# Kernel tuning notes

Hardware: AMD Instinct MI355X
Metric: run time of the kernel (lower is better)

The kernel has to match this reference:

```python
import jax, jax.numpy as jnp
import numpy as np

NUM_HEADS = 12


def setup_inputs() -> dict:
    key = jax.random.key(0)
    ks = jax.random.split(key, 12)
    B, S, H = 8, 1024, 768
    h = jax.random.normal(ks[0], (B, S, H), dtype=jnp.float32)
    att_bias = jax.random.normal(ks[1], (B, S, S, NUM_HEADS), dtype=jnp.float32)
    mask = jax.random.randint(ks[2], (B, S, S), 0, 2, dtype=jnp.int32)
    sc = 1.0 / np.sqrt(H)
    Wq = jax.random.normal(ks[3], (H, H), dtype=jnp.float32) * sc
    bq = jax.random.normal(ks[4], (H,), dtype=jnp.float32) * 0.01
    Wk = jax.random.normal(ks[5], (H, H), dtype=jnp.float32) * sc
    bk = jax.random.normal(ks[6], (H,), dtype=jnp.float32) * 0.01
    Wv = jax.random.normal(ks[7], (H, H), dtype=jnp.float32) * sc
    bv = jax.random.normal(ks[8], (H,), dtype=jnp.float32) * 0.01
    Wo = jax.random.normal(ks[9], (H, H), dtype=jnp.float32) * sc
    bo = jax.random.normal(ks[10], (H,), dtype=jnp.float32) * 0.01
    return {"h": h, "att_bias": att_bias, "mask": mask,
            "Wq": Wq, "bq": bq, "Wk": Wk, "bk": bk,
            "Wv": Wv, "bv": bv, "Wo": Wo, "bo": bo}


def reference(h, att_bias, mask, Wq, bq, Wk, bk, Wv, bv, Wo, bo):
    B, S, H = h.shape
    nh = NUM_HEADS
    d = H // nh
    scale = d ** -0.5
    # projections -> [B, nh, S, d]
    q = (h @ Wq + bq).reshape(B, S, nh, d).transpose(0, 2, 1, 3)
    k = (h @ Wk + bk).reshape(B, S, nh, d).transpose(0, 2, 1, 3)
    v = (h @ Wv + bv).reshape(B, S, nh, d).transpose(0, 2, 1, 3)
    # scores [B, nh, S, S] + additive bias (permuted from [B,S,S,nh])
    scores = jnp.einsum('bhqd,bhkd->bhqk', q, k) * scale
    scores = scores + att_bias.transpose(0, 3, 1, 2)
    # masked_fill with 1e-14 (faithful to original: near-zero score, not -inf)
    scores = jnp.where(mask[:, None, :, :].astype(bool),
                       jnp.asarray(1e-14, scores.dtype), scores)
    attn = jax.nn.softmax(scores, axis=-1)  # dropout p=0 -> identity
    out = jnp.einsum('bhqk,bhkd->bhqd', attn, v)
    out = out.transpose(0, 2, 1, 3).reshape(B, S, H)
    return out @ Wo + bo
```

## Files before the change

kernel.cpp:

```cpp
#include <hip/hip_runtime.h>


typedef __attribute__((ext_vector_type(8))) __bf16 bf16x8;
typedef __attribute__((ext_vector_type(4))) __bf16 bf16x4;
typedef __attribute__((ext_vector_type(4))) float floatx4;
typedef __attribute__((ext_vector_type(4))) short short4v;
using bf16 = __bf16;

#define HID 768
#define NHEAD 12
#define DHEAD 64
#define SEQ 1024
#define NBATCH 8
#define WELEM (HID * HID)
#define QKVELEM (NBATCH * NHEAD * SEQ * DHEAD)
#define OPELEM QKVELEM
#define MLROWS (NBATCH * NHEAD * SEQ)

__device__ __forceinline__ floatx4 mfma_bf16(bf16x8 a, bf16x8 b, floatx4 c) {
  return __builtin_amdgcn_mfma_f32_16x16x32_bf16(a, b, c, 0, 0, 0);
}

__device__ __forceinline__ floatx4 mfma16_bf16(bf16x4 a, bf16x4 b, floatx4 c) {
#if __has_builtin(__builtin_amdgcn_mfma_f32_16x16x16bf16_1k)
  return __builtin_amdgcn_mfma_f32_16x16x16bf16_1k(
      __builtin_bit_cast(short4v, a), __builtin_bit_cast(short4v, b), c, 0, 0, 0);
#else
  floatx4 d = c;
  asm volatile("s_nop 1\n\tv_mfma_f32_16x16x16_bf16 %0, %1, %2, %0\n\ts_nop 4"
               : "+v"(d) : "v"(a), "v"(b));
  return d;
#endif
}

#define ASYNC16(gp, lp)                                           \
  __builtin_amdgcn_global_load_lds(                               \
      (__attribute__((address_space(1))) void*)(gp),              \
      (__attribute__((address_space(3))) void*)(lp), 16, 0, 0)

__global__ void prep_weights(const float* __restrict__ Wq, const float* __restrict__ Wk,
                             const float* __restrict__ Wv, const float* __restrict__ Wo,
                             bf16* __restrict__ WT) {
  __shared__ float t[32][33];
  const int m = blockIdx.z;
  const float* W = (m == 0) ? Wq : (m == 1) ? Wk : (m == 2) ? Wv : Wo;
  const int k0 = blockIdx.x * 32, n0 = blockIdx.y * 32;
  const int tx = threadIdx.x, ty = threadIdx.y;
#pragma unroll
  for (int i = 0; i < 4; ++i)
    t[ty + 8 * i][tx] = W[(size_t)(k0 + ty + 8 * i) * HID + n0 + tx];
  __syncthreads();
  bf16* o = WT + (size_t)m * WELEM;
#pragma unroll
  for (int i = 0; i < 4; ++i)
    o[(size_t)(n0 + ty + 8 * i) * HID + k0 + tx] = (bf16)t[tx][ty + 8 * i];
}

__global__ void prep_h(const float* __restrict__ X, bf16* __restrict__ Y) {
  const size_t i = ((size_t)blockIdx.x * 256 + threadIdx.x) * 8;
  float4 a = *(const float4*)(X + i);
  float4 b = *(const float4*)(X + i + 4);
  bf16x8 o;
  o[0] = (bf16)a.x; o[1] = (bf16)a.y; o[2] = (bf16)a.z; o[3] = (bf16)a.w;
  o[4] = (bf16)b.x; o[5] = (bf16)b.y; o[6] = (bf16)b.z; o[7] = (bf16)b.w;
  *(bf16x8*)(Y + i) = o;
}

__launch_bounds__(256, 2)
__global__ void qkv_gemm(const bf16* __restrict__ A, const bf16* __restrict__ WT,
                         const float* __restrict__ bq, const float* __restrict__ bk,
                         const float* __restrict__ bv,
                         bf16* __restrict__ Qb, bf16* __restrict__ Kb,
                         bf16* __restrict__ Vb) {
  __shared__ __align__(16) bf16 As[128][32];
  __shared__ __align__(16) bf16 Bs[128][32];
  const int mat = blockIdx.z;
  const int bn = blockIdx.x * 128, bm = blockIdx.y * 128;
  const bf16* W = WT + (size_t)mat * WELEM;
  const int tid = threadIdx.x, lane = tid & 63, warp = tid >> 6;
  const int fr = lane & 15, quad = lane >> 4;
  const int wr = warp >> 1, wc = warp & 1;

  floatx4 acc[4][4] = {};

  const int srow = tid >> 2, scol = (tid & 3) * 8;
  const bf16* as0 = A + (size_t)(bm + srow) * HID + scol;
  const bf16* as1 = A + (size_t)(bm + 64 + srow) * HID + scol;
  const bf16* bs0 = W + (size_t)(bn + srow) * HID + scol;
  const bf16* bs1 = W + (size_t)(bn + 64 + srow) * HID + scol;
  bf16* la0 = &As[srow][scol];
  bf16* la1 = &As[64 + srow][scol];
  bf16* lb0 = &Bs[srow][scol];
  bf16* lb1 = &Bs[64 + srow][scol];

  for (int k0 = 0; k0 < HID; k0 += 32) {
    ASYNC16(as0 + k0, la0);
    ASYNC16(as1 + k0, la1);
    ASYNC16(bs0 + k0, lb0);
    ASYNC16(bs1 + k0, lb1);
    __syncthreads();
    bf16x8 a[4], b[4];
#pragma unroll
    for (int mi = 0; mi < 4; ++mi) a[mi] = *(const bf16x8*)&As[wr * 64 + mi * 16 + fr][quad * 8];
#pragma unroll
    for (int ni = 0; ni < 4; ++ni) b[ni] = *(const bf16x8*)&Bs[wc * 64 + ni * 16 + fr][quad * 8];
#pragma unroll
    for (int mi = 0; mi < 4; ++mi)
#pragma unroll
      for (int ni = 0; ni < 4; ++ni) acc[mi][ni] = mfma_bf16(a[mi], b[ni], acc[mi][ni]);
    __syncthreads();
  }

  const float* bias = (mat == 0) ? bq : (mat == 1) ? bk : bv;
#pragma unroll
  for (int mi = 0; mi < 4; ++mi)
#pragma unroll
    for (int ni = 0; ni < 4; ++ni)
#pragma unroll
      for (int r = 0; r < 4; ++r) {
        const int grow = bm + wr * 64 + mi * 16 + quad * 4 + r;
        const int gcol = bn + wc * 64 + ni * 16 + fr;
        float v = acc[mi][ni][r] + bias[gcol];
        const int bb = grow >> 10, ss = grow & 1023;
        const int head = gcol >> 6, dc = gcol & 63;
        const size_t bh = (size_t)bb * NHEAD + head;
        const size_t idx = (bh * SEQ + ss) * DHEAD + dc;
        if (mat == 0) Qb[idx] = (bf16)(v * 0.125f);
        else if (mat == 1) Kb[idx] = (bf16)v;
        else Vb[idx] = (bf16)v;
      }
}

__global__ void vtrans(const bf16* __restrict__ Vb, bf16* __restrict__ Vt) {
  __shared__ bf16 t[64][72];
  const int st = blockIdx.x, bh = blockIdx.y;
  const int tid = threadIdx.x;
  const bf16* src = Vb + ((size_t)bh * SEQ + st * 64) * DHEAD;
#pragma unroll
  for (int p = 0; p < 2; ++p) {
    const int r = p * 32 + (tid >> 3), c = (tid & 7) * 8;
    *(bf16x8*)&t[r][c] = *(const bf16x8*)(src + (size_t)r * DHEAD + c);
  }
  __syncthreads();
#pragma unroll
  for (int p = 0; p < 2; ++p) {
    const int d = p * 32 + (tid >> 3), s0 = (tid & 7) * 8;
    bf16x8 o;
#pragma unroll
    for (int k = 0; k < 8; ++k) o[k] = t[s0 + k][d];
    *(bf16x8*)(Vt + ((size_t)bh * DHEAD + d) * SEQ + st * 64 + s0) = o;
  }
}

__launch_bounds__(256, 4)
__global__ void attn_kernel(const bf16* __restrict__ Qb, const bf16* __restrict__ Kb,
                            const bf16* __restrict__ Vt, const float* __restrict__ bias,
                            const int* __restrict__ maskp,
                            float* __restrict__ Op, float2* __restrict__ Ml) {
  __shared__ __align__(16) float4 BbU[1536];
  __shared__ __align__(16) int4  MbU[128];

  const int qt = blockIdx.x, b = blockIdx.y, ks = blockIdx.z;
  const int tid = threadIdx.x, lane = tid & 63, warp = tid >> 6;
  const int fr = lane & 15, quad = lane >> 4;
  const size_t brow = (size_t)b * SEQ + qt * 16;

  float* Opk = Op + (size_t)ks * OPELEM;
  float2* Mlk = Ml + (size_t)ks * MLROWS;

  bf16x8 qa0[3], qa1[3];
#pragma unroll
  for (int j = 0; j < 3; ++j) {
    const size_t bh = (size_t)b * NHEAD + 3 * warp + j;
    const bf16* Qp = Qb + (bh * SEQ + qt * 16) * DHEAD;
    qa0[j] = *(const bf16x8*)(Qp + fr * DHEAD + quad * 8);
    qa1[j] = *(const bf16x8*)(Qp + fr * DHEAD + 32 + quad * 8);
  }

  const float4* bias4 = (const float4*)bias;
  const float4* bsrc[6];
#pragma unroll
  for (int i = 0; i < 6; ++i) {
    const int f = tid + 256 * i, q = f / 96, rl = f % 96;
    const int rg = (rl & ~7) | ((rl ^ q) & 7);
    bsrc[i] = bias4 + ((size_t)(brow + q) * SEQ) * 3 + rg;
  }
  const int4* msrc = nullptr;
  if (tid < 128) {
    const int q = tid >> 3, s = tid & 7;
    msrc = (const int4*)(maskp + (size_t)(brow + q) * SEQ) + (s ^ (q & 7));
  }

  float mrun[3] = {-1e30f, -1e30f, -1e30f};
  float lrun[3] = {0.f, 0.f, 0.f};
  floatx4 oaccT[3][4] = {};

  for (int ch = 0; ch < 16; ++ch) {
    const int c0 = (ks * 16 + ch) * 32;

#pragma unroll
    for (int i = 0; i < 6; ++i) ASYNC16(bsrc[i] + c0 * 3, BbU + tid + 256 * i);
    if (tid < 128) ASYNC16(msrc + c0 / 4, MbU + tid);
    __syncthreads();

    floatx4 st[3][2];
#pragma unroll
    for (int j = 0; j < 3; ++j) {
      const size_t bh = (size_t)b * NHEAD + 3 * warp + j;
#pragma unroll
      for (int ct = 0; ct < 2; ++ct) {
        const bf16* kp = Kb + (bh * SEQ + c0 + ct * 16 + fr) * DHEAD;
        bf16x8 k0 = *(const bf16x8*)(kp + quad * 8);
        bf16x8 k1 = *(const bf16x8*)(kp + 32 + quad * 8);
        floatx4 t = {0.f, 0.f, 0.f, 0.f};
        t = mfma_bf16(k0, qa0[j], t);
        t = mfma_bf16(k1, qa1[j], t);
        st[j][ct] = t;
      }
    }

    const float* Bf = (const float*)BbU;
#pragma unroll
    for (int ct = 0; ct < 2; ++ct) {
      const int4 m4 = MbU[fr * 8 + ((ct * 4 + quad) ^ (fr & 7))];
      const int mm[4] = {m4.x, m4.y, m4.z, m4.w};
#pragma unroll
      for (int r = 0; r < 4; ++r) {
        const int ug = 3 * (ct * 16 + quad * 4 + r);
        const int u0 = fr * 96 + ((ug & ~7) | ((ug ^ fr) & 7));
        const int u1 = fr * 96 + (((ug + 1) & ~7) | (((ug + 1) ^ fr) & 7));
        const int u2 = fr * 96 + (((ug + 2) & ~7) | (((ug + 2) ^ fr) & 7));
        float b0, b1, b2;
        if (warp == 0)      { const float* p = Bf + 4 * u0; b0 = p[0]; b1 = p[1]; b2 = p[2]; }
        else if (warp == 1) { const float* p = Bf + 4 * u1; b0 = Bf[4 * u0 + 3]; b1 = p[0]; b2 = p[1]; }
        else if (warp == 2) { const float* p = Bf + 4 * u1; b0 = p[2]; b1 = p[3]; b2 = Bf[4 * u2]; }
        else                { const float* p = Bf + 4 * u2; b0 = p[1]; b1 = p[2]; b2 = p[3]; }
        if (mm[r]) {
          st[0][ct][r] = 0.f; st[1][ct][r] = 0.f; st[2][ct][r] = 0.f;
        } else {
          st[0][ct][r] += b0; st[1][ct][r] += b1; st[2][ct][r] += b2;
        }
      }
    }

#pragma unroll
    for (int j = 0; j < 3; ++j) {
      float s8[8];
#pragma unroll
      for (int ct = 0; ct < 2; ++ct)
#pragma unroll
        for (int r = 0; r < 4; ++r) s8[ct * 4 + r] = st[j][ct][r];
      float mx = mrun[j];
#pragma unroll
      for (int k = 0; k < 8; ++k) mx = fmaxf(mx, s8[k]);
      mx = fmaxf(mx, __shfl_xor(mx, 16));
      mx = fmaxf(mx, __shfl_xor(mx, 32));
      const float alpha = __expf(mrun[j] - mx);
      float e[8], sum = 0.f;
#pragma unroll
      for (int k = 0; k < 8; ++k) { e[k] = __expf(s8[k] - mx); sum += e[k]; }
      sum += __shfl_xor(sum, 16);
      sum += __shfl_xor(sum, 32);
      lrun[j] = lrun[j] * alpha + sum;
      mrun[j] = mx;
      bf16x4 pa0, pa1;
#pragma unroll
      for (int r = 0; r < 4; ++r) { pa0[r] = (bf16)e[r]; pa1[r] = (bf16)e[4 + r]; }
#pragma unroll
      for (int dvt = 0; dvt < 4; ++dvt)
#pragma unroll
        for (int r = 0; r < 4; ++r) oaccT[j][dvt][r] *= alpha;
      const size_t bh = (size_t)b * NHEAD + 3 * warp + j;
#pragma unroll
      for (int dvt = 0; dvt < 4; ++dvt) {
        const bf16* vp = Vt + (bh * DHEAD + dvt * 16 + fr) * SEQ + c0 + quad * 4;
        bf16x4 v0 = *(const bf16x4*)vp;
        bf16x4 v1 = *(const bf16x4*)(vp + 16);
        oaccT[j][dvt] = mfma16_bf16(v0, pa0, oaccT[j][dvt]);
        oaccT[j][dvt] = mfma16_bf16(v1, pa1, oaccT[j][dvt]);
      }
    }

    __syncthreads();
  }

#pragma unroll
  for (int j = 0; j < 3; ++j) {
    const int hh = 3 * warp + j;
    const size_t row = ((size_t)b * NHEAD + hh) * SEQ + qt * 16 + fr;
#pragma unroll
    for (int dvt = 0; dvt < 4; ++dvt)
      *(floatx4*)(Opk + row * DHEAD + dvt * 16 + quad * 4) = oaccT[j][dvt];
    if (quad == 0) Mlk[row] = make_float2(mrun[j], lrun[j]);
  }
}

__global__ void kmerge(const float* __restrict__ O0, const float* __restrict__ O1,
                       const float2* __restrict__ ml0, const float2* __restrict__ ml1,
                       bf16* __restrict__ Ob) {
  const int t = blockIdx.x * 256 + threadIdx.x;
  const int row = t >> 4;
  const int dq = (t & 15) * 4;
  const float2 a = ml0[row], c = ml1[row];
  const float M = fmaxf(a.x, c.x);
  const float w0 = __expf(a.x - M), w1 = __expf(c.x - M);
  const float inv = 1.0f / (a.y * w0 + c.y * w1);
  floatx4 o0 = *(const floatx4*)(O0 + (size_t)row * DHEAD + dq);
  floatx4 o1 = *(const floatx4*)(O1 + (size_t)row * DHEAD + dq);
  const int bh = row >> 10, s = row & 1023;
  const int bb = bh / NHEAD, hh = bh % NHEAD;
  bf16x4 o;
#pragma unroll
  for (int r = 0; r < 4; ++r) o[r] = (bf16)((o0[r] * w0 + o1[r] * w1) * inv);
  *(bf16x4*)(Ob + ((size_t)bb * SEQ + s) * HID + hh * DHEAD + dq) = o;
}

__launch_bounds__(256, 2)
__global__ void out_gemm(const bf16* __restrict__ A, const bf16* __restrict__ W,
                         const float* __restrict__ bo, float* __restrict__ out) {
  __shared__ __align__(16) bf16 As[128][32];
  __shared__ __align__(16) bf16 Bs[128][32];
  const int bn = blockIdx.x * 128, bm = blockIdx.y * 128;
  const int tid = threadIdx.x, lane = tid & 63, warp = tid >> 6;
  const int fr = lane & 15, quad = lane >> 4;
  const int wr = warp >> 1, wc = warp & 1;

  floatx4 acc[4][4] = {};

  const int srow = tid >> 2, scol = (tid & 3) * 8;
  const bf16* as0 = A + (size_t)(bm + srow) * HID + scol;
  const bf16* as1 = A + (size_t)(bm + 64 + srow) * HID + scol;
  const bf16* bs0 = W + (size_t)(bn + srow) * HID + scol;
  const bf16* bs1 = W + (size_t)(bn + 64 + srow) * HID + scol;
  bf16* la0 = &As[srow][scol];
  bf16* la1 = &As[64 + srow][scol];
  bf16* lb0 = &Bs[srow][scol];
  bf16* lb1 = &Bs[64 + srow][scol];

  for (int k0 = 0; k0 < HID; k0 += 32) {
    ASYNC16(as0 + k0, la0);
    ASYNC16(as1 + k0, la1);
    ASYNC16(bs0 + k0, lb0);
    ASYNC16(bs1 + k0, lb1);
    __syncthreads();
    bf16x8 a[4], b[4];
#pragma unroll
    for (int mi = 0; mi < 4; ++mi) a[mi] = *(const bf16x8*)&As[wr * 64 + mi * 16 + fr][quad * 8];
#pragma unroll
    for (int ni = 0; ni < 4; ++ni) b[ni] = *(const bf16x8*)&Bs[wc * 64 + ni * 16 + fr][quad * 8];
#pragma unroll
    for (int mi = 0; mi < 4; ++mi)
#pragma unroll
      for (int ni = 0; ni < 4; ++ni) acc[mi][ni] = mfma_bf16(a[mi], b[ni], acc[mi][ni]);
    __syncthreads();
  }

#pragma unroll
  for (int mi = 0; mi < 4; ++mi)
#pragma unroll
    for (int ni = 0; ni < 4; ++ni)
#pragma unroll
      for (int r = 0; r < 4; ++r) {
        const int grow = bm + wr * 64 + mi * 16 + quad * 4 + r;
        const int gcol = bn + wc * 64 + ni * 16 + fr;
        out[(size_t)grow * HID + gcol] = acc[mi][ni][r] + bo[gcol];
      }
}

extern "C" void kernel_launch(void* const* d_in, const int* in_sizes, int n_in,
                              void* d_out, int out_size, void* d_ws, size_t ws_size,
                              hipStream_t stream) {
  const float* h  = (const float*)d_in[0];
  const float* ab = (const float*)d_in[1];
  const int*   mk = (const int*)d_in[2];
  const float* Wq = (const float*)d_in[3];
  const float* bq = (const float*)d_in[4];
  const float* Wk = (const float*)d_in[5];
  const float* bk = (const float*)d_in[6];
  const float* Wv = (const float*)d_in[7];
  const float* bv = (const float*)d_in[8];
  const float* Wo = (const float*)d_in[9];
  const float* bo = (const float*)d_in[10];
  float* out = (float*)d_out;

  bf16* WT = (bf16*)d_ws;
  bf16* hb = WT + (size_t)4 * WELEM;
  bf16* Qb = hb + (size_t)QKVELEM;
  bf16* Kb = Qb + (size_t)QKVELEM;
  bf16* Vb = Kb + (size_t)QKVELEM;
  bf16* Vt = Vb + (size_t)QKVELEM;
  bf16* Ob = Vb;
  float* Opw = (float*)(Vt + (size_t)QKVELEM);
  float2* Mlw = (float2*)(Opw + (size_t)2 * OPELEM);

  prep_weights<<<dim3(24, 24, 4), dim3(32, 8), 0, stream>>>(Wq, Wk, Wv, Wo, WT);
  prep_h<<<3072, 256, 0, stream>>>(h, hb);
  qkv_gemm<<<dim3(6, 64, 3), 256, 0, stream>>>(hb, WT, bq, bk, bv, Qb, Kb, Vb);
  vtrans<<<dim3(16, 96), 256, 0, stream>>>(Vb, Vt);
  attn_kernel<<<dim3(64, 8, 2), 256, 0, stream>>>(Qb, Kb, Vt, ab, mk, Opw, Mlw);
  kmerge<<<6144, 256, 0, stream>>>(Opw, Opw + OPELEM, Mlw, Mlw + MLROWS, Ob);
  out_gemm<<<dim3(6, 64), 256, 0, stream>>>(Ob, WT + (size_t)3 * WELEM, bo, out);
}
```

Measured before the change: 980.9 us.

## Restructure attention: one head per warp, bitpacked mask, double-buffered bias, drop split-K merge

The attention kernel now gives each warp a single head, with a block covering 4 heads of a 16-query tile. It runs over the full key range, which removes the two-way key split, the fp32 partial outputs and the kmerge kernel. Each block reads only its head group's bias slice, double-buffered with async copies so the next chunk overlaps compute. The int32 mask is packed into bitwords by a new kernel and loaded once per block. V is stored in a permuted layout so each lane does one 16-byte load instead of two 8-byte loads. In exchange, each query's mask and bias rows are now fetched by three blocks instead of one, the grid shape changes, and launch bounds are raised to 6 blocks per CU.

```diff
diff --git a/kernel.cpp b/kernel.cpp
--- a/kernel.cpp
+++ b/kernel.cpp
@@ -14,8 +14,6 @@
 #define NBATCH 8
 #define WELEM (HID * HID)
 #define QKVELEM (NBATCH * NHEAD * SEQ * DHEAD)
-#define OPELEM QKVELEM
-#define MLROWS (NBATCH * NHEAD * SEQ)
 
 __device__ __forceinline__ floatx4 mfma_bf16(bf16x8 a, bf16x8 b, floatx4 c) {
   return __builtin_amdgcn_mfma_f32_16x16x32_bf16(a, b, c, 0, 0, 0);
@@ -64,6 +62,21 @@
   o[0] = (bf16)a.x; o[1] = (bf16)a.y; o[2] = (bf16)a.z; o[3] = (bf16)a.w;
   o[4] = (bf16)b.x; o[5] = (bf16)b.y; o[6] = (bf16)b.z; o[7] = (bf16)b.w;
   *(bf16x8*)(Y + i) = o;
+}
+
+__global__ void maskpack(const int* __restrict__ mp, unsigned int* __restrict__ Mb) {
+  const size_t t = (size_t)blockIdx.x * 256 + threadIdx.x;
+  const int4* src = (const int4*)(mp + t * 32);
+  unsigned int bits = 0u;
+#pragma unroll
+  for (int i = 0; i < 8; ++i) {
+    int4 m = src[i];
+    bits |= (m.x ? 1u : 0u) << (4 * i);
+    bits |= (m.y ? 1u : 0u) << (4 * i + 1);
+    bits |= (m.z ? 1u : 0u) << (4 * i + 2);
+    bits |= (m.w ? 1u : 0u) << (4 * i + 3);
+  }
+  Mb[t] = bits;
 }
 
 __launch_bounds__(256, 2)
@@ -131,7 +144,7 @@
       }
 }
 
-__global__ void vtrans(const bf16* __restrict__ Vb, bf16* __restrict__ Vt) {
+__global__ void vtrans(const bf16* __restrict__ Vb, bf16* __restrict__ Vp) {
   __shared__ bf16 t[64][72];
   const int st = blockIdx.x, bh = blockIdx.y;
   const int tid = threadIdx.x;
@@ -144,175 +157,135 @@
   __syncthreads();
 #pragma unroll
   for (int p = 0; p < 2; ++p) {
-    const int d = p * 32 + (tid >> 3), s0 = (tid & 7) * 8;
+    const int d = p * 32 + (tid >> 3);
+    const int p0 = (tid & 7) * 8;
+    const int cb = p0 & ~31;
+    const int g = (p0 >> 3) & 3;
     bf16x8 o;
 #pragma unroll
-    for (int k = 0; k < 8; ++k) o[k] = t[s0 + k][d];
-    *(bf16x8*)(Vt + ((size_t)bh * DHEAD + d) * SEQ + st * 64 + s0) = o;
-  }
-}
-
-__launch_bounds__(256, 4)
+    for (int j = 0; j < 8; ++j) {
+      const int k = cb + ((j < 4) ? (g * 4 + j) : (16 + g * 4 + (j - 4)));
+      o[j] = t[k][d];
+    }
+    *(bf16x8*)(Vp + ((size_t)bh * DHEAD + d) * SEQ + st * 64 + p0) = o;
+  }
+}
+
+__launch_bounds__(256, 6)
 __global__ void attn_kernel(const bf16* __restrict__ Qb, const bf16* __restrict__ Kb,
-                            const bf16* __restrict__ Vt, const float* __restrict__ bias,
-                            const int* __restrict__ maskp,
-                            float* __restrict__ Op, float2* __restrict__ Ml) {
-  __shared__ __align__(16) float4 BbU[1536];
-  __shared__ __align__(16) int4  MbU[128];
-
-  const int qt = blockIdx.x, b = blockIdx.y, ks = blockIdx.z;
+                            const bf16* __restrict__ Vp, const float* __restrict__ bias,
+                            const unsigned int* __restrict__ Mbits,
+                            bf16* __restrict__ Ob) {
+  __shared__ __align__(16) float4 Bb[2][512];
+  __shared__ __align__(16) int4 Mw[128];
+
+  const int blk = blockIdx.x;
+  const int b = blk & 7;
+  const int t2 = blk >> 3;
+  const int hg = t2 % 3, qt = t2 / 3;
+
   const int tid = threadIdx.x, lane = tid & 63, warp = tid >> 6;
-  const int fr = lane & 15, quad = lane >> 4;
+  const int fr = lane & 15, quad = lane >> 4, f7 = fr & 7;
   const size_t brow = (size_t)b * SEQ + qt * 16;
-
-  float* Opk = Op + (size_t)ks * OPELEM;
-  float2* Mlk = Ml + (size_t)ks * MLROWS;
-
-  bf16x8 qa0[3], qa1[3];
-#pragma unroll
-  for (int j = 0; j < 3; ++j) {
-    const size_t bh = (size_t)b * NHEAD + 3 * warp + j;
-    const bf16* Qp = Qb + (bh * SEQ + qt * 16) * DHEAD;
-    qa0[j] = *(const bf16x8*)(Qp + fr * DHEAD + quad * 8);
-    qa1[j] = *(const bf16x8*)(Qp + fr * DHEAD + 32 + quad * 8);
-  }
+  const int h = hg * 4 + warp;
+  const size_t bh = (size_t)b * NHEAD + h;
+
+  const bf16* Qp = Qb + (bh * SEQ + qt * 16) * DHEAD;
+  const bf16x8 qa0 = *(const bf16x8*)(Qp + fr * DHEAD + quad * 8);
+  const bf16x8 qa1 = *(const bf16x8*)(Qp + fr * DHEAD + 32 + quad * 8);
 
   const float4* bias4 = (const float4*)bias;
-  const float4* bsrc[6];
-#pragma unroll
-  for (int i = 0; i < 6; ++i) {
-    const int f = tid + 256 * i, q = f / 96, rl = f % 96;
-    const int rg = (rl & ~7) | ((rl ^ q) & 7);
-    bsrc[i] = bias4 + ((size_t)(brow + q) * SEQ) * 3 + rg;
-  }
-  const int4* msrc = nullptr;
+  const int p0 = tid, p1 = tid + 256;
+  const int q0s = p0 >> 5, k0s = (p0 & 31) ^ (q0s & 7);
+  const int q1s = p1 >> 5, k1s = (p1 & 31) ^ (q1s & 7);
+  const float4* bsrc0 = bias4 + ((size_t)(brow + q0s) * SEQ + k0s) * 3 + hg;
+  const float4* bsrc1 = bias4 + ((size_t)(brow + q1s) * SEQ + k1s) * 3 + hg;
+
+  ASYNC16(bsrc0, &Bb[0][p0]);
+  ASYNC16(bsrc1, &Bb[0][p1]);
   if (tid < 128) {
-    const int q = tid >> 3, s = tid & 7;
-    msrc = (const int4*)(maskp + (size_t)(brow + q) * SEQ) + (s ^ (q & 7));
-  }
-
-  float mrun[3] = {-1e30f, -1e30f, -1e30f};
-  float lrun[3] = {0.f, 0.f, 0.f};
-  floatx4 oaccT[3][4] = {};
-
-  for (int ch = 0; ch < 16; ++ch) {
-    const int c0 = (ks * 16 + ch) * 32;
-
-#pragma unroll
-    for (int i = 0; i < 6; ++i) ASYNC16(bsrc[i] + c0 * 3, BbU + tid + 256 * i);
-    if (tid < 128) ASYNC16(msrc + c0 / 4, MbU + tid);
-    __syncthreads();
-
-    floatx4 st[3][2];
-#pragma unroll
-    for (int j = 0; j < 3; ++j) {
-      const size_t bh = (size_t)b * NHEAD + 3 * warp + j;
-#pragma unroll
-      for (int ct = 0; ct < 2; ++ct) {
-        const bf16* kp = Kb + (bh * SEQ + c0 + ct * 16 + fr) * DHEAD;
-        bf16x8 k0 = *(const bf16x8*)(kp + quad * 8);
-        bf16x8 k1 = *(const bf16x8*)(kp + 32 + quad * 8);
-        floatx4 t = {0.f, 0.f, 0.f, 0.f};
-        t = mfma_bf16(k0, qa0[j], t);
-        t = mfma_bf16(k1, qa1[j], t);
-        st[j][ct] = t;
+    const int mq = tid >> 3, mu = (tid & 7) ^ (mq & 7);
+    ASYNC16((const int4*)(Mbits + (size_t)(brow + mq) * 32) + mu, &Mw[tid]);
+  }
+  __syncthreads();
+
+  const unsigned int* Mwords = (const unsigned int*)Mw;
+  float mrun = -1e30f, lrun = 0.f;
+  floatx4 oacc[4] = {};
+
+  for (int ch = 0; ch < 32; ++ch) {
+    const int c0 = ch * 32;
+
+    if (ch < 31) {
+      float4* Bn = Bb[(ch + 1) & 1];
+      ASYNC16(bsrc0 + (ch + 1) * 96, Bn + p0);
+      ASYNC16(bsrc1 + (ch + 1) * 96, Bn + p1);
+    }
+
+    floatx4 st[2];
+#pragma unroll
+    for (int ct = 0; ct < 2; ++ct) {
+      const bf16* kp = Kb + (bh * SEQ + c0 + ct * 16 + fr) * DHEAD;
+      bf16x8 kf0 = *(const bf16x8*)(kp + quad * 8);
+      bf16x8 kf1 = *(const bf16x8*)(kp + 32 + quad * 8);
+      floatx4 t = {0.f, 0.f, 0.f, 0.f};
+      t = mfma_bf16(kf0, qa0, t);
+      t = mfma_bf16(kf1, qa1, t);
+      st[ct] = t;
+    }
+
+    const float* Bf = (const float*)Bb[ch & 1];
+    const unsigned int mword = Mwords[(fr << 5) + (ch ^ (f7 << 2))];
+    float s8[8];
+#pragma unroll
+    for (int ct = 0; ct < 2; ++ct)
+#pragma unroll
+      for (int r = 0; r < 4; ++r) {
+        const int k = ct * 16 + quad * 4 + r;
+        const float bv = Bf[((fr << 5) + (k ^ f7)) * 4 + warp];
+        s8[ct * 4 + r] = ((mword >> k) & 1u) ? 0.f : (st[ct][r] + bv);
       }
+
+    float mx = mrun;
+#pragma unroll
+    for (int k = 0; k < 8; ++k) mx = fmaxf(mx, s8[k]);
+    mx = fmaxf(mx, __shfl_xor(mx, 16));
+    mx = fmaxf(mx, __shfl_xor(mx, 32));
+    const float alpha = __expf(mrun - mx);
+    float e[8], sum = 0.f;
+#pragma unroll
+    for (int k = 0; k < 8; ++k) { e[k] = __expf(s8[k] - mx); sum += e[k]; }
+    sum += __shfl_xor(sum, 16);
+    sum += __shfl_xor(sum, 32);
+    lrun = lrun * alpha + sum;
+    mrun = mx;
+    bf16x4 pa0, pa1;
+#pragma unroll
+    for (int r = 0; r < 4; ++r) { pa0[r] = (bf16)e[r]; pa1[r] = (bf16)e[4 + r]; }
+
+#pragma unroll
+    for (int dvt = 0; dvt < 4; ++dvt) {
+#pragma unroll
+      for (int r = 0; r < 4; ++r) oacc[dvt][r] *= alpha;
+      const bf16* vp = Vp + (bh * DHEAD + dvt * 16 + fr) * SEQ + c0 + quad * 8;
+      bf16x8 vv = *(const bf16x8*)vp;
+      bf16x4 v0 = {vv[0], vv[1], vv[2], vv[3]};
+      bf16x4 v1 = {vv[4], vv[5], vv[6], vv[7]};
+      oacc[dvt] = mfma16_bf16(v0, pa0, oacc[dvt]);
+      oacc[dvt] = mfma16_bf16(v1, pa1, oacc[dvt]);
     }
 
-    const float* Bf = (const float*)BbU;
-#pragma unroll
-    for (int ct = 0; ct < 2; ++ct) {
-      const int4 m4 = MbU[fr * 8 + ((ct * 4 + quad) ^ (fr & 7))];
-      const int mm[4] = {m4.x, m4.y, m4.z, m4.w};
-#pragma unroll
-      for (int r = 0; r < 4; ++r) {
-        const int ug = 3 * (ct * 16 + quad * 4 + r);
-        const int u0 = fr * 96 + ((ug & ~7) | ((ug ^ fr) & 7));
-        const int u1 = fr * 96 + (((ug + 1) & ~7) | (((ug + 1) ^ fr) & 7));
-        const int u2 = fr * 96 + (((ug + 2) & ~7) | (((ug + 2) ^ fr) & 7));
-        float b0, b1, b2;
-        if (warp == 0)      { const float* p = Bf + 4 * u0; b0 = p[0]; b1 = p[1]; b2 = p[2]; }
-        else if (warp == 1) { const float* p = Bf + 4 * u1; b0 = Bf[4 * u0 + 3]; b1 = p[0]; b2 = p[1]; }
-        else if (warp == 2) { const float* p = Bf + 4 * u1; b0 = p[2]; b1 = p[3]; b2 = Bf[4 * u2]; }
-        else                { const float* p = Bf + 4 * u2; b0 = p[1]; b1 = p[2]; b2 = p[3]; }
-        if (mm[r]) {
-          st[0][ct][r] = 0.f; st[1][ct][r] = 0.f; st[2][ct][r] = 0.f;
-        } else {
-          st[0][ct][r] += b0; st[1][ct][r] += b1; st[2][ct][r] += b2;
-        }
-      }
-    }
-
-#pragma unroll
-    for (int j = 0; j < 3; ++j) {
-      float s8[8];
-#pragma unroll
-      for (int ct = 0; ct < 2; ++ct)
-#pragma unroll
-        for (int r = 0; r < 4; ++r) s8[ct * 4 + r] = st[j][ct][r];
-      float mx = mrun[j];
-#pragma unroll
-      for (int k = 0; k < 8; ++k) mx = fmaxf(mx, s8[k]);
-      mx = fmaxf(mx, __shfl_xor(mx, 16));
-      mx = fmaxf(mx, __shfl_xor(mx, 32));
-      const float alpha = __expf(mrun[j] - mx);
-      float e[8], sum = 0.f;
-#pragma unroll
-      for (int k = 0; k < 8; ++k) { e[k] = __expf(s8[k] - mx); sum += e[k]; }
-      sum += __shfl_xor(sum, 16);
-      sum += __shfl_xor(sum, 32);
-      lrun[j] = lrun[j] * alpha + sum;
-      mrun[j] = mx;
-      bf16x4 pa0, pa1;
-#pragma unroll
-      for (int r = 0; r < 4; ++r) { pa0[r] = (bf16)e[r]; pa1[r] = (bf16)e[4 + r]; }
-#pragma unroll
-      for (int dvt = 0; dvt < 4; ++dvt)
-#pragma unroll
-        for (int r = 0; r < 4; ++r) oaccT[j][dvt][r] *= alpha;
-      const size_t bh = (size_t)b * NHEAD + 3 * warp + j;
-#pragma unroll
-      for (int dvt = 0; dvt < 4; ++dvt) {
-        const bf16* vp = Vt + (bh * DHEAD + dvt * 16 + fr) * SEQ + c0 + quad * 4;
-        bf16x4 v0 = *(const bf16x4*)vp;
-        bf16x4 v1 = *(const bf16x4*)(vp + 16);
-        oaccT[j][dvt] = mfma16_bf16(v0, pa0, oaccT[j][dvt]);
-        oaccT[j][dvt] = mfma16_bf16(v1, pa1, oaccT[j][dvt]);
-      }
-    }
-
-    __syncthreads();
-  }
-
-#pragma unroll
-  for (int j = 0; j < 3; ++j) {
-    const int hh = 3 * warp + j;
-    const size_t row = ((size_t)b * NHEAD + hh) * SEQ + qt * 16 + fr;
-#pragma unroll
-    for (int dvt = 0; dvt < 4; ++dvt)
-      *(floatx4*)(Opk + row * DHEAD + dvt * 16 + quad * 4) = oaccT[j][dvt];
-    if (quad == 0) Mlk[row] = make_float2(mrun[j], lrun[j]);
-  }
-}
-
-__global__ void kmerge(const float* __restrict__ O0, const float* __restrict__ O1,
-                       const float2* __restrict__ ml0, const float2* __restrict__ ml1,
-                       bf16* __restrict__ Ob) {
-  const int t = blockIdx.x * 256 + threadIdx.x;
-  const int row = t >> 4;
-  const int dq = (t & 15) * 4;
-  const float2 a = ml0[row], c = ml1[row];
-  const float M = fmaxf(a.x, c.x);
-  const float w0 = __expf(a.x - M), w1 = __expf(c.x - M);
-  const float inv = 1.0f / (a.y * w0 + c.y * w1);
-  floatx4 o0 = *(const floatx4*)(O0 + (size_t)row * DHEAD + dq);
-  floatx4 o1 = *(const floatx4*)(O1 + (size_t)row * DHEAD + dq);
-  const int bh = row >> 10, s = row & 1023;
-  const int bb = bh / NHEAD, hh = bh % NHEAD;
-  bf16x4 o;
-#pragma unroll
-  for (int r = 0; r < 4; ++r) o[r] = (bf16)((o0[r] * w0 + o1[r] * w1) * inv);
-  *(bf16x4*)(Ob + ((size_t)bb * SEQ + s) * HID + hh * DHEAD + dq) = o;
+    __syncthreads();
+  }
+
+  const float linv = 1.0f / lrun;
+#pragma unroll
+  for (int dvt = 0; dvt < 4; ++dvt) {
+    bf16x4 o;
+#pragma unroll
+    for (int r = 0; r < 4; ++r) o[r] = (bf16)(oacc[dvt][r] * linv);
+    *(bf16x4*)(Ob + (brow + fr) * HID + h * 64 + dvt * 16 + quad * 4) = o;
+  }
 }
 
 __launch_bounds__(256, 2)
@@ -388,16 +361,15 @@
   bf16* Qb = hb + (size_t)QKVELEM;
   bf16* Kb = Qb + (size_t)QKVELEM;
   bf16* Vb = Kb + (size_t)QKVELEM;
-  bf16* Vt = Vb + (size_t)QKVELEM;
+  bf16* Vp = Vb + (size_t)QKVELEM;
   bf16* Ob = Vb;
-  float* Opw = (float*)(Vt + (size_t)QKVELEM);
-  float2* Mlw = (float2*)(Opw + (size_t)2 * OPELEM);
+  unsigned int* Mbits = (unsigned int*)(Vp + (size_t)QKVELEM);
 
   prep_weights<<<dim3(24, 24, 4), dim3(32, 8), 0, stream>>>(Wq, Wk, Wv, Wo, WT);
   prep_h<<<3072, 256, 0, stream>>>(h, hb);
+  maskpack<<<1024, 256, 0, stream>>>(mk, Mbits);
   qkv_gemm<<<dim3(6, 64, 3), 256, 0, stream>>>(hb, WT, bq, bk, bv, Qb, Kb, Vb);
-  vtrans<<<dim3(16, 96), 256, 0, stream>>>(Vb, Vt);
-  attn_kernel<<<dim3(64, 8, 2), 256, 0, stream>>>(Qb, Kb, Vt, ab, mk, Opw, Mlw);
-  kmerge<<<6144, 256, 0, stream>>>(Opw, Opw + OPELEM, Mlw, Mlw + MLROWS, Ob);
+  vtrans<<<dim3(16, 96), 256, 0, stream>>>(Vb, Vp);
+  attn_kernel<<<1536, 256, 0, stream>>>(Qb, Kb, Vp, ab, Mbits, Ob);
   out_gemm<<<dim3(6, 64), 256, 0, stream>>>(Ob, WT + (size_t)3 * WELEM, bo, out);
 }
```

Measured after the change: 798.6 us. -18.6%, faster.
